# Kernel tuning notes

Measured on AMD Instinct MI355X. Metric: run time of the kernel, lower is better.

The kernel has to match this reference:

```python
import jax, jax.numpy as jnp
import numpy as np

N, HID, L, NC = 2048, 256, 4, 10
D0, D1, D2 = HID, HID // 2, HID // 8   # dims for degrees l=0,1,2
H, DH = 4, HID // 4                    # heads for degree-0 attention
F = D0 + D1 + D2                       # invariant feature width
C2 = float(np.sqrt(3.0))


def setup_inputs() -> dict:
    key = jax.random.key(0)
    ks = jax.random.split(key, 16)

    def w(k, shape, fan):
        return jax.random.normal(k, shape, jnp.float32) / np.float32(np.sqrt(fan))

    return {
        "x": jax.random.uniform(ks[0], (N, 118), jnp.float32),
        "pos": jax.random.normal(ks[1], (N, 3), jnp.float32) * 3.0,
        "emb_W": w(ks[2], (118, D0), 118),
        "emb_b": jnp.zeros((D0,), jnp.float32),
        "Wq": w(ks[3], (L, F, H * DH), F),
        "Wk": w(ks[4], (L, F, H * DH), F),
        "Wv0": w(ks[5], (L, D0, D0), D0),
        "Wv1": w(ks[6], (L, D1, D1), D1),
        "Wv2": w(ks[7], (L, D2, D2), D2),
        "Ws1": w(ks[8], (L, D0, D1), D0),
        "Ws2": w(ks[9], (L, D0, D2), D0),
        "Wffa": w(ks[10], (L, D0, 2 * D0), D0),
        "Wffb": w(ks[11], (L, 2 * D0, D0), 2 * D0),
        "Wg": w(ks[12], (L, F, D1 + D2), F),
        "out_W": w(ks[13], (D0, NC), D0),
        "out_b": jnp.zeros((NC,), jnp.float32),
    }


def _sph_harmonics(pos):
    """Real spherical harmonics Y1 [N,N,3], Y2 [N,N,5] of pairwise unit vectors."""
    rel = pos[None, :, :] - pos[:, None, :]                  # [N,N,3]
    dist = jnp.linalg.norm(rel, axis=-1, keepdims=True)
    valid = (dist > 1e-6).astype(pos.dtype)                  # zero out self-pairs
    u = rel / jnp.maximum(dist, 1e-6) * valid
    ux, uy, uz = u[..., 0], u[..., 1], u[..., 2]
    Y1 = u
    Y2 = jnp.stack([
        C2 * ux * uy,
        C2 * uy * uz,
        0.5 * (3.0 * uz * uz - 1.0),
        C2 * ux * uz,
        0.5 * C2 * (ux * ux - uy * uy),
    ], axis=-1) * valid                                      # [N,N,5]
    return Y1, Y2


def _invariants(x0, x1, x2):
    return jnp.concatenate([
        x0,
        jnp.linalg.norm(x1, axis=-1),
        jnp.linalg.norm(x2, axis=-1),
    ], axis=-1)                                              # [N,F]


def _layer(x0, x1, x2, Y1, Y2, Wq, Wk, Wv0, Wv1, Wv2, Ws1, Ws2, Wffa, Wffb, Wg):
    inv = _invariants(x0, x1, x2)
    q = (inv @ Wq).reshape(N, H, DH)
    k = (inv @ Wk).reshape(N, H, DH)
    attn = jax.nn.softmax(jnp.einsum('nhd,mhd->hnm', q, k) / np.float32(np.sqrt(DH)), axis=-1)

    # degree-0 aggregation (4 heads)
    v0 = (x0 @ Wv0).reshape(N, H, D0 // H)
    agg0 = jnp.einsum('hnm,mhc->nhc', attn, v0).reshape(N, D0)

    a = attn.mean(0)                                         # [N,N] single head for l>0
    # degree-1: channel-mixed values + degree-0 -> degree-1 via Y1
    v1 = jnp.einsum('mdc,de->mec', x1, Wv1)                  # [N,D1,3]
    agg1 = jnp.einsum('nm,mdc->ndc', a, v1)
    mix1 = jnp.einsum('nmc,md->ndc', a[:, :, None] * Y1, x0 @ Ws1)
    # degree-2: channel-mixed values + degree-0 -> degree-2 via Y2
    v2 = jnp.einsum('mdc,de->mec', x2, Wv2)                  # [N,D2,5]
    agg2 = jnp.einsum('nm,mdc->ndc', a, v2)
    mix2 = jnp.einsum('nmc,md->ndc', a[:, :, None] * Y2, x0 @ Ws2)

    x0 = x0 + agg0
    x1 = x1 + agg1 + mix1
    x2 = x2 + agg2 + mix2

    # gated equivariant feedforward
    x0 = x0 + jax.nn.silu(x0 @ Wffa) @ Wffb
    g = jax.nn.sigmoid(_invariants(x0, x1, x2) @ Wg)         # [N,D1+D2]
    x1 = x1 * g[:, :D1, None]
    x2 = x2 * g[:, D1:, None]
    return x0, x1, x2


def reference(x, pos, emb_W, emb_b, Wq, Wk, Wv0, Wv1, Wv2, Ws1, Ws2, Wffa, Wffb, Wg, out_W, out_b):
    Y1, Y2 = _sph_harmonics(pos)
    x0 = x @ emb_W + emb_b                                   # input embedding
    x1 = jnp.zeros((N, D1, 3), x0.dtype)
    x2 = jnp.zeros((N, D2, 5), x0.dtype)
    for l in range(L):
        x0, x1, x2 = _layer(x0, x1, x2, Y1, Y2,
                            Wq[l], Wk[l], Wv0[l], Wv1[l], Wv2[l],
                            Ws1[l], Ws2[l], Wffa[l], Wffb[l], Wg[l])
    return x0 @ out_W + out_b                                # [N, num_classes]
```

## Files before the change

kernel.cpp:

```cpp
#include <hip/hip_runtime.h>
#include <math.h>

#define N_    2048
#define D0_   256
#define D1_   128
#define D2_   32
#define F_    416
#define H_    4
#define DH_   64
#define L_    4
#define NC_   10
#define C2_   1.7320508075688772f
#define X12W  544

typedef unsigned short u16;
typedef __attribute__((ext_vector_type(8))) short short8v;
typedef __attribute__((ext_vector_type(4))) float f32x4;

union U8 { u16 u[8]; short8v v; };

__device__ __forceinline__ u16 f2bf(float f) {
    union { float f; unsigned int u; } x; x.f = f;
    unsigned int r = x.u + 0x7FFFu + ((x.u >> 16) & 1u);
    return (u16)(r >> 16);
}
__device__ __forceinline__ float bf2f(u16 u) {
    union { float f; unsigned int u; } x; x.u = ((unsigned int)u) << 16;
    return x.f;
}

__device__ __forceinline__ f32x4 mfma16(short8v a, short8v b, f32x4 c) {
    return __builtin_amdgcn_mfma_f32_16x16x32_bf16(a, b, c, 0, 0, 0);
}

enum { B_NN = 0, B_NT = 1 };
enum { EPI_STORE = 0, EPI_SILU = 1, EPI_SIGMOID = 2, EPI_ACCUM = 3, EPI_ATOMIC = 4,
       EPI_STOREB = 5 };

template<int BLAY, int EPI>
__global__ __launch_bounds__(256) void mfma_gemm(
    const float* __restrict__ A, int lda,
    const float* __restrict__ B, int ldb,
    const float* __restrict__ bias,
    float* __restrict__ C, int ldc,
    int M, int K, int Nn, float scale, int kchunk,
    int zk, long long Ah, long long Bh, long long Ch)
{
    __shared__ __align__(16) u16 As[64][40];
    __shared__ __align__(16) u16 Bs[64][40];
    const int t = threadIdx.x;
    const int bm = blockIdx.y * 64, bn = blockIdx.x * 64;
    const int hz = blockIdx.z / zk, kz = blockIdx.z % zk;
    A += (size_t)hz * Ah; B += (size_t)hz * Bh;
    const int lane = t & 63, w = t >> 6;
    const int r0 = (w >> 1) * 32, c0 = (w & 1) * 32;
    const int fr = lane & 15, fk = (lane >> 4) * 8;
    const int ml = t >> 2, k8 = (t & 3) * 8;
    const int kbeg = kz * kchunk;
    const int kend = (kbeg + kchunk < K) ? kbeg + kchunk : K;
    f32x4 acc[2][2] = {};

    for (int k0 = kbeg; k0 < kend; k0 += 32) {
        {
            U8 u;
            if (((lda & 3) == 0) && (k0 + 32 <= kend)) {
                const float* ap = A + (size_t)(bm + ml) * lda + k0 + k8;
                float4 a0 = *(const float4*)ap;
                float4 a1 = *(const float4*)(ap + 4);
                u.u[0]=f2bf(a0.x); u.u[1]=f2bf(a0.y); u.u[2]=f2bf(a0.z); u.u[3]=f2bf(a0.w);
                u.u[4]=f2bf(a1.x); u.u[5]=f2bf(a1.y); u.u[6]=f2bf(a1.z); u.u[7]=f2bf(a1.w);
            } else {
#pragma unroll
                for (int j = 0; j < 8; ++j) {
                    int kk = k0 + k8 + j;
                    u.u[j] = f2bf(kk < kend ? A[(size_t)(bm + ml) * lda + kk] : 0.f);
                }
            }
            *(short8v*)&As[ml][k8] = u.v;
        }
        {
            U8 u;
            if (BLAY == B_NT) {
                if (((ldb & 3) == 0) && (k0 + 32 <= kend) && (bn + ml < Nn)) {
                    const float* bp = B + (size_t)(bn + ml) * ldb + k0 + k8;
                    float4 b0 = *(const float4*)bp;
                    float4 b1 = *(const float4*)(bp + 4);
                    u.u[0]=f2bf(b0.x); u.u[1]=f2bf(b0.y); u.u[2]=f2bf(b0.z); u.u[3]=f2bf(b0.w);
                    u.u[4]=f2bf(b1.x); u.u[5]=f2bf(b1.y); u.u[6]=f2bf(b1.z); u.u[7]=f2bf(b1.w);
                } else {
#pragma unroll
                    for (int j = 0; j < 8; ++j) {
                        int kk = k0 + k8 + j;
                        u.u[j] = f2bf((kk < kend && bn + ml < Nn)
                                      ? B[(size_t)(bn + ml) * ldb + kk] : 0.f);
                    }
                }
            } else {
                int nc = bn + ml;
#pragma unroll
                for (int j = 0; j < 8; ++j) {
                    int kk = k0 + k8 + j;
                    u.u[j] = f2bf((kk < kend && nc < Nn) ? B[(size_t)kk * ldb + nc] : 0.f);
                }
            }
            *(short8v*)&Bs[ml][k8] = u.v;
        }
        __syncthreads();
        short8v a0 = *(const short8v*)&As[r0 + fr][fk];
        short8v a1 = *(const short8v*)&As[r0 + 16 + fr][fk];
        short8v b0 = *(const short8v*)&Bs[c0 + fr][fk];
        short8v b1 = *(const short8v*)&Bs[c0 + 16 + fr][fk];
        acc[0][0] = mfma16(a0, b0, acc[0][0]);
        acc[0][1] = mfma16(a0, b1, acc[0][1]);
        acc[1][0] = mfma16(a1, b0, acc[1][0]);
        acc[1][1] = mfma16(a1, b1, acc[1][1]);
        __syncthreads();
    }
#pragma unroll
    for (int mi = 0; mi < 2; ++mi)
#pragma unroll
    for (int ni = 0; ni < 2; ++ni)
#pragma unroll
    for (int r = 0; r < 4; ++r) {
        int row = bm + r0 + mi * 16 + ((lane >> 4) << 2) + r;
        int col = bn + c0 + ni * 16 + fr;
        if (col >= Nn) continue;
        float v = acc[mi][ni][r];
        if (EPI == EPI_STOREB) {
            ((u16*)C + (size_t)hz * Ch)[(size_t)row * ldc + col] = f2bf(v * scale);
        } else {
            float* cp = C + (size_t)hz * Ch + (size_t)row * ldc + col;
            if (EPI == EPI_STORE)   *cp = v * scale + (bias ? bias[col] : 0.f);
            if (EPI == EPI_SILU)    *cp = v / (1.f + expf(-v));
            if (EPI == EPI_SIGMOID) *cp = 1.f / (1.f + expf(-v));
            if (EPI == EPI_ACCUM)   *cp += v;
            if (EPI == EPI_ATOMIC)  atomicAdd(cp, v);
        }
    }
}

template<int NB, int EPI>
__global__ __launch_bounds__(256) void aggP(
    const u16* __restrict__ A, int lda,
    const float* __restrict__ B, int ldb,
    float* __restrict__ C, int ldc,
    int K, int Nn, int kchunk,
    int zk, long long Ah, long long Bh, long long Ch)
{
    __shared__ __align__(16) u16 As[64][40];
    __shared__ __align__(16) u16 Bs[NB][64][40];
    const int t = threadIdx.x;
    const int bm = blockIdx.y * 64, bn0 = blockIdx.x * 64 * NB;
    const int hz = blockIdx.z / zk, kz = blockIdx.z % zk;
    A += (size_t)hz * Ah; B += (size_t)hz * Bh; C += (size_t)hz * Ch;
    const int lane = t & 63, w = t >> 6;
    const int r0 = (w >> 1) * 32, c0 = (w & 1) * 32;
    const int fr = lane & 15, fk = (lane >> 4) * 8;
    const int ml = t >> 2, k8 = (t & 3) * 8;
    const int kbeg = kz * kchunk;
    const int kend = (kbeg + kchunk < K) ? kbeg + kchunk : K;
    f32x4 acc[NB][2][2] = {};

    for (int k0 = kbeg; k0 < kend; k0 += 32) {
        *(short8v*)&As[ml][k8] = *(const short8v*)(A + (size_t)(bm + ml) * lda + k0 + k8);
#pragma unroll
        for (int nb = 0; nb < NB; ++nb) {
            int nc = bn0 + nb * 64 + ml;
            U8 u;
#pragma unroll
            for (int j = 0; j < 8; ++j) {
                int kk = k0 + k8 + j;
                u.u[j] = f2bf(nc < Nn ? B[(size_t)kk * ldb + nc] : 0.f);
            }
            *(short8v*)&Bs[nb][ml][k8] = u.v;
        }
        __syncthreads();
        short8v a0 = *(const short8v*)&As[r0 + fr][fk];
        short8v a1 = *(const short8v*)&As[r0 + 16 + fr][fk];
#pragma unroll
        for (int nb = 0; nb < NB; ++nb) {
            short8v b0 = *(const short8v*)&Bs[nb][c0 + fr][fk];
            short8v b1 = *(const short8v*)&Bs[nb][c0 + 16 + fr][fk];
            acc[nb][0][0] = mfma16(a0, b0, acc[nb][0][0]);
            acc[nb][0][1] = mfma16(a0, b1, acc[nb][0][1]);
            acc[nb][1][0] = mfma16(a1, b0, acc[nb][1][0]);
            acc[nb][1][1] = mfma16(a1, b1, acc[nb][1][1]);
        }
        __syncthreads();
    }
#pragma unroll
    for (int nb = 0; nb < NB; ++nb)
#pragma unroll
    for (int mi = 0; mi < 2; ++mi)
#pragma unroll
    for (int ni = 0; ni < 2; ++ni)
#pragma unroll
    for (int r = 0; r < 4; ++r) {
        int row = bm + r0 + mi * 16 + ((lane >> 4) << 2) + r;
        int col = bn0 + nb * 64 + c0 + ni * 16 + fr;
        if (col >= Nn) continue;
        float v = acc[nb][mi][ni][r];
        float* cp = C + (size_t)row * ldc + col;
        if (EPI == EPI_ATOMIC) atomicAdd(cp, v);
        else                   *cp += v;
    }
}

__global__ void ucompute_kernel(const float* __restrict__ pos, u16* __restrict__ U) {
    int idx = blockIdx.x * 256 + threadIdx.x;
    int n = idx >> 11, m = idx & (N_ - 1);
    float rx = pos[m * 3 + 0] - pos[n * 3 + 0];
    float ry = pos[m * 3 + 1] - pos[n * 3 + 1];
    float rz = pos[m * 3 + 2] - pos[n * 3 + 2];
    float d2 = rx * rx + ry * ry + rz * rz;
    bool valid = d2 > 1e-12f;
    float rinv = valid ? rsqrtf(d2) : 0.f;
    size_t base = (size_t)n * N_ + m;
    const size_t CS = (size_t)N_ * N_;
    U[base]          = f2bf(rx * rinv);
    U[base + CS]     = f2bf(ry * rinv);
    U[base + 2 * CS] = f2bf(rz * rinv);
}

__global__ __launch_bounds__(256) void mixc_kernel(
    const u16* __restrict__ amb, const u16* __restrict__ U,
    const float* __restrict__ s1, const float* __restrict__ s2,
    float* __restrict__ x12)
{
    const int ch = blockIdx.z;
    const int gx = blockIdx.x;
    const int bm = blockIdx.y * 64;
    const size_t CS = (size_t)N_ * N_;
    const bool deg1 = ch < 3;
    const int colbase = deg1 ? (gx & 1) * 64 : 0;
    const int ks      = deg1 ? (gx >> 1) : gx;
    const int kchunk  = deg1 ? 512 : 256;
    const float* Bp   = deg1 ? s1 : s2;
    const int Bld     = deg1 ? 128 : 32;
    __shared__ __align__(16) u16 As[64][40];
    __shared__ __align__(16) u16 Bs[64][40];
    const int t = threadIdx.x, lane = t & 63, w = t >> 6;
    const int r0 = (w >> 1) * 32, c0 = (w & 1) * 32;
    const int fr = lane & 15, fk = (lane >> 4) * 8;
    const int ml = t >> 2, k8 = (t & 3) * 8;
    const int kbeg = ks * kchunk, kend = kbeg + kchunk;
    f32x4 acc[2][2] = {};

    for (int m0 = kbeg; m0 < kend; m0 += 32) {
        const size_t off = (size_t)(bm + ml) * N_ + m0 + k8;
        U8 am8; am8.v = *(const short8v*)(amb + off);
        U8 o;
        if (deg1) {
            U8 uv; uv.v = *(const short8v*)(U + (size_t)ch * CS + off);
#pragma unroll
            for (int j = 0; j < 8; ++j)
                o.u[j] = f2bf(bf2f(am8.u[j]) * bf2f(uv.u[j]));
        } else {
            U8 xv, yv, zv;
            xv.v = *(const short8v*)(U + off);
            yv.v = *(const short8v*)(U + CS + off);
            zv.v = *(const short8v*)(U + 2 * CS + off);
#pragma unroll
            for (int j = 0; j < 8; ++j) {
                float a = bf2f(am8.u[j]);
                float ux = bf2f(xv.u[j]), uy = bf2f(yv.u[j]), uz = bf2f(zv.u[j]);
                float y;
                if      (ch == 3) y = C2_ * ux * uy;
                else if (ch == 4) y = C2_ * uy * uz;
                else if (ch == 5) y = (ux*ux + uy*uy + uz*uz > 0.5f)
                                      ? 0.5f * (3.f * uz * uz - 1.f) : 0.f;
                else if (ch == 6) y = C2_ * ux * uz;
                else              y = 0.5f * C2_ * (ux * ux - uy * uy);
                o.u[j] = f2bf(a * y);
            }
        }
        *(short8v*)&As[ml][k8] = o.v;
        {
            int nc = colbase + ml;
            U8 u;
#pragma unroll
            for (int j = 0; j < 8; ++j)
                u.u[j] = f2bf((deg1 || nc < 32)
                              ? Bp[(size_t)(m0 + k8 + j) * Bld + nc] : 0.f);
            *(short8v*)&Bs[ml][k8] = u.v;
        }
        __syncthreads();
        short8v a0 = *(const short8v*)&As[r0 + fr][fk];
        short8v a1 = *(const short8v*)&As[r0 + 16 + fr][fk];
        short8v b0 = *(const short8v*)&Bs[c0 + fr][fk];
        short8v b1 = *(const short8v*)&Bs[c0 + 16 + fr][fk];
        acc[0][0] = mfma16(a0, b0, acc[0][0]);
        acc[0][1] = mfma16(a0, b1, acc[0][1]);
        acc[1][0] = mfma16(a1, b0, acc[1][0]);
        acc[1][1] = mfma16(a1, b1, acc[1][1]);
        __syncthreads();
    }
#pragma unroll
    for (int mi = 0; mi < 2; ++mi)
#pragma unroll
    for (int ni = 0; ni < 2; ++ni)
#pragma unroll
    for (int r = 0; r < 4; ++r) {
        int row = bm + r0 + mi * 16 + ((lane >> 4) << 2) + r;
        int col = colbase + c0 + ni * 16 + fr;
        float v = acc[mi][ni][r];
        if (deg1)          atomicAdd(&x12[(size_t)row * X12W + col * 3 + ch], v);
        else if (col < 32) atomicAdd(&x12[(size_t)row * X12W + 384 + col * 5 + (ch - 3)], v);
    }
}

__global__ void invar_kernel(const float* __restrict__ x0, const float* __restrict__ x12,
                             float* __restrict__ inv) {
    int n = blockIdx.x, t = threadIdx.x;
    inv[(size_t)n * F_ + t] = x0[(size_t)n * D0_ + t];
    if (t < 128) {
        const float* p = x12 + (size_t)n * X12W + t * 3;
        inv[(size_t)n * F_ + 256 + t] = sqrtf(p[0]*p[0] + p[1]*p[1] + p[2]*p[2]);
    }
    if (t < 32) {
        const float* p = x12 + (size_t)n * X12W + 384 + t * 5;
        inv[(size_t)n * F_ + 384 + t] =
            sqrtf(p[0]*p[0] + p[1]*p[1] + p[2]*p[2] + p[3]*p[3] + p[4]*p[4]);
    }
}

__global__ void v1_kernel(const float* __restrict__ x12, const float* __restrict__ W,
                          float* __restrict__ Vflat) {
    int m = blockIdx.x, t = threadIdx.x;
    __shared__ float sh[384];
    sh[t] = x12[(size_t)m * X12W + t];
    __syncthreads();
    int e = t / 3, c = t % 3;
    float acc = 0.f;
#pragma unroll 4
    for (int d = 0; d < 128; ++d)
        acc = fmaf(sh[d * 3 + c], W[d * 128 + e], acc);
    Vflat[(size_t)m * X12W + t] = acc;
}

__global__ void v2_kernel(const float* __restrict__ x12, const float* __restrict__ W,
                          float* __restrict__ Vflat) {
    int m = blockIdx.x, t = threadIdx.x;
    __shared__ float sh[160];
    if (t < 160) sh[t] = x12[(size_t)m * X12W + 384 + t];
    __syncthreads();
    if (t < 160) {
        int e = t / 5, c = t % 5;
        float acc = 0.f;
#pragma unroll 4
        for (int d = 0; d < 32; ++d)
            acc = fmaf(sh[d * 5 + c], W[d * 32 + e], acc);
        Vflat[(size_t)m * X12W + 384 + t] = acc;
    }
}

__global__ void softmax4(u16* __restrict__ Sb, u16* __restrict__ amb) {
    int n = blockIdx.x, t = threadIdx.x;
    __shared__ float red[256];
    const size_t NN = (size_t)N_ * N_;
    float amv[8] = {};
    for (int h = 0; h < H_; ++h) {
        u16* Sp = Sb + (size_t)h * NN + (size_t)n * N_ + t * 8;
        U8 sv; sv.v = *(const short8v*)Sp;
        float s[8];
#pragma unroll
        for (int j = 0; j < 8; ++j) s[j] = bf2f(sv.u[j]);
        float mx = s[0];
#pragma unroll
        for (int j = 1; j < 8; ++j) mx = fmaxf(mx, s[j]);
        red[t] = mx; __syncthreads();
        for (int st = 128; st > 0; st >>= 1) { if (t < st) red[t] = fmaxf(red[t], red[t + st]); __syncthreads(); }
        mx = red[0]; __syncthreads();
        float sum = 0.f;
#pragma unroll
        for (int j = 0; j < 8; ++j) { s[j] = expf(s[j] - mx); sum += s[j]; }
        red[t] = sum; __syncthreads();
        for (int st = 128; st > 0; st >>= 1) { if (t < st) red[t] += red[t + st]; __syncthreads(); }
        float rinv = 1.f / red[0]; __syncthreads();
        U8 pv;
#pragma unroll
        for (int j = 0; j < 8; ++j) {
            float p = s[j] * rinv;
            pv.u[j] = f2bf(p);
            amv[j] += 0.25f * p;
        }
        *(short8v*)Sp = pv.v;
    }
    U8 av;
#pragma unroll
    for (int j = 0; j < 8; ++j) av.u[j] = f2bf(amv[j]);
    *(short8v*)(amb + (size_t)n * N_ + t * 8) = av.v;
}

__global__ void gate_kernel(const float* __restrict__ g, float* __restrict__ x12) {
    int idx = blockIdx.x * 256 + threadIdx.x;
    if (idx >= N_ * X12W) return;
    int n = idx / X12W, j = idx % X12W;
    float gv = (j < 384) ? g[n * 160 + j / 3] : g[n * 160 + 128 + (j - 384) / 5];
    x12[idx] *= gv;
}

extern "C" void kernel_launch(void* const* d_in, const int* in_sizes, int n_in,
                              void* d_out, int out_size, void* d_ws, size_t ws_size,
                              hipStream_t stream) {
    const float* x    = (const float*)d_in[0];
    const float* pos  = (const float*)d_in[1];
    const float* embW = (const float*)d_in[2];
    const float* embB = (const float*)d_in[3];
    const float* Wq   = (const float*)d_in[4];
    const float* Wk   = (const float*)d_in[5];
    const float* Wv0  = (const float*)d_in[6];
    const float* Wv1  = (const float*)d_in[7];
    const float* Wv2  = (const float*)d_in[8];
    const float* Ws1  = (const float*)d_in[9];
    const float* Ws2  = (const float*)d_in[10];
    const float* Wffa = (const float*)d_in[11];
    const float* Wffb = (const float*)d_in[12];
    const float* Wg   = (const float*)d_in[13];
    const float* outW = (const float*)d_in[14];
    const float* outB = (const float*)d_in[15];
    float* out = (float*)d_out;

    const size_t NN = (size_t)N_ * N_;
    float* p = (float*)d_ws;
    float* x0    = p; p += N_ * D0_;
    float* x12   = p; p += N_ * X12W;
    float* inv   = p; p += N_ * F_;
    float* q     = p; p += N_ * D0_;
    float* k     = p; p += N_ * D0_;
    float* v0    = p; p += N_ * D0_;
    float* Vflat = p; p += N_ * X12W;
    float* s1    = p; p += N_ * D1_;
    float* s2    = p; p += N_ * D2_;
    float* fft   = p; p += N_ * 512;
    float* gm    = p; p += N_ * 160;
    u16* ub  = (u16*)p;
    u16* Sb  = ub; ub += 4 * NN;
    u16* amb = ub; ub += NN;
    u16* U   = ub;

    hipMemsetAsync(x12, 0, (size_t)N_ * X12W * sizeof(float), stream);
    ucompute_kernel<<<(N_ * N_) / 256, 256, 0, stream>>>(pos, U);

    mfma_gemm<B_NN, EPI_STORE><<<dim3(4, 32), 256, 0, stream>>>(
        x, 118, embW, 256, embB, x0, 256, N_, 118, 256, 1.f, 118, 1, 0, 0, 0);

    for (int l = 0; l < L_; ++l) {
        const float* Wq_l   = Wq   + (size_t)l * F_ * 256;
        const float* Wk_l   = Wk   + (size_t)l * F_ * 256;
        const float* Wv0_l  = Wv0  + (size_t)l * 256 * 256;
        const float* Wv1_l  = Wv1  + (size_t)l * 128 * 128;
        const float* Wv2_l  = Wv2  + (size_t)l * 32 * 32;
        const float* Ws1_l  = Ws1  + (size_t)l * 256 * 128;
        const float* Ws2_l  = Ws2  + (size_t)l * 256 * 32;
        const float* Wffa_l = Wffa + (size_t)l * 256 * 512;
        const float* Wffb_l = Wffb + (size_t)l * 512 * 256;
        const float* Wg_l   = Wg   + (size_t)l * F_ * 160;

        invar_kernel<<<N_, 256, 0, stream>>>(x0, x12, inv);
        mfma_gemm<B_NN, EPI_STORE><<<dim3(4, 32), 256, 0, stream>>>(
            inv, F_, Wq_l, 256, nullptr, q, 256, N_, F_, 256, 1.f, F_, 1, 0, 0, 0);
        mfma_gemm<B_NN, EPI_STORE><<<dim3(4, 32), 256, 0, stream>>>(
            inv, F_, Wk_l, 256, nullptr, k, 256, N_, F_, 256, 1.f, F_, 1, 0, 0, 0);
        mfma_gemm<B_NN, EPI_STORE><<<dim3(4, 32), 256, 0, stream>>>(
            x0, 256, Wv0_l, 256, nullptr, v0, 256, N_, 256, 256, 1.f, 256, 1, 0, 0, 0);
        mfma_gemm<B_NN, EPI_STORE><<<dim3(2, 32), 256, 0, stream>>>(
            x0, 256, Ws1_l, 128, nullptr, s1, 128, N_, 256, 128, 1.f, 256, 1, 0, 0, 0);
        mfma_gemm<B_NN, EPI_STORE><<<dim3(1, 32), 256, 0, stream>>>(
            x0, 256, Ws2_l, 32, nullptr, s2, 32, N_, 256, 32, 1.f, 256, 1, 0, 0, 0);
        v1_kernel<<<N_, 384, 0, stream>>>(x12, Wv1_l, Vflat);
        v2_kernel<<<N_, 192, 0, stream>>>(x12, Wv2_l, Vflat);

        mfma_gemm<B_NT, EPI_STOREB><<<dim3(32, 32, 4), 256, 0, stream>>>(
            q, 256, k, 256, nullptr, (float*)Sb, N_, N_, 64, N_, 0.125f, 64,
            1, 64, 64, (long long)NN);
        softmax4<<<N_, 256, 0, stream>>>(Sb, amb);
        aggP<1, EPI_ATOMIC><<<dim3(1, 32, 32), 256, 0, stream>>>(
            Sb, N_, v0, 256, x0, 256, N_, 64, 256,
            8, (long long)NN, 64, 64);

        aggP<3, EPI_ATOMIC><<<dim3(3, 32, 4), 256, 0, stream>>>(
            amb, N_, Vflat, X12W, x12, X12W, N_, X12W, 512,
            4, 0, 0, 0);
        mixc_kernel<<<dim3(8, 32, 8), 256, 0, stream>>>(amb, U, s1, s2, x12);

        mfma_gemm<B_NN, EPI_SILU><<<dim3(8, 32), 256, 0, stream>>>(
            x0, 256, Wffa_l, 512, nullptr, fft, 512, N_, 256, 512, 1.f, 256, 1, 0, 0, 0);
        mfma_gemm<B_NN, EPI_ACCUM><<<dim3(4, 32), 256, 0, stream>>>(
            fft, 512, Wffb_l, 256, nullptr, x0, 256, N_, 512, 256, 1.f, 512, 1, 0, 0, 0);

        invar_kernel<<<N_, 256, 0, stream>>>(x0, x12, inv);
        mfma_gemm<B_NN, EPI_SIGMOID><<<dim3(3, 32), 256, 0, stream>>>(
            inv, F_, Wg_l, 160, nullptr, gm, 160, N_, F_, 160, 1.f, F_, 1, 0, 0, 0);
        gate_kernel<<<(N_ * X12W + 255) / 256, 256, 0, stream>>>(gm, x12);
    }

    mfma_gemm<B_NN, EPI_STORE><<<dim3(1, 32), 256, 0, stream>>>(
        x0, 256, outW, NC_, outB, out, NC_, N_, 256, NC_, 1.f, 256, 1, 0, 0, 0);
}
```

Before: 1.569 ms.

## Pre-transpose B operands to bf16 and stage mix results in contiguous accumulators

Adds a bf16 transpose kernel so the aggregation and mix GEMMs load their B tiles as contiguous 16-byte vectors instead of eight strided fp32 loads with per-element conversion. The mix kernel now writes atomics to a channel-separated contiguous buffer rather than strided interleaved x12 slots, then a combine kernel adds that buffer into x12. The degree-1 mix grid is also split further along K (16 x-blocks, 256-wide chunks). The cost is extra transpose, memset and combine launches plus more atomic traffic from the finer K split.

```diff
diff --git a/kernel.cpp b/kernel.cpp
--- a/kernel.cpp
+++ b/kernel.cpp
@@ -139,10 +139,30 @@
     }
 }
 
-template<int NB, int EPI>
+__global__ __launch_bounds__(256) void transpose_bf16(
+    const float* __restrict__ in, u16* __restrict__ outT, int R, int C)
+{
+    __shared__ float tile[64][65];
+    const int br = blockIdx.y * 64, bc = blockIdx.x * 64;
+    const int t = threadIdx.x, lc = t & 63, q = t >> 6;
+#pragma unroll 4
+    for (int r = 0; r < 16; ++r) {
+        int row = br + q * 16 + r, col = bc + lc;
+        tile[q * 16 + r][lc] = (col < C) ? in[(size_t)row * C + col] : 0.f;
+    }
+    __syncthreads();
+#pragma unroll 4
+    for (int r = 0; r < 16; ++r) {
+        int orow = bc + q * 16 + r;
+        int ocol = br + lc;
+        if (orow < C) outT[(size_t)orow * R + ocol] = f2bf(tile[lc][q * 16 + r]);
+    }
+}
+
+template<int NB>
 __global__ __launch_bounds__(256) void aggP(
     const u16* __restrict__ A, int lda,
-    const float* __restrict__ B, int ldb,
+    const u16* __restrict__ BT, int ldk,
     float* __restrict__ C, int ldc,
     int K, int Nn, int kchunk,
     int zk, long long Ah, long long Bh, long long Ch)
@@ -152,7 +172,7 @@
     const int t = threadIdx.x;
     const int bm = blockIdx.y * 64, bn0 = blockIdx.x * 64 * NB;
     const int hz = blockIdx.z / zk, kz = blockIdx.z % zk;
-    A += (size_t)hz * Ah; B += (size_t)hz * Bh; C += (size_t)hz * Ch;
+    A += (size_t)hz * Ah; BT += (size_t)hz * Bh; C += (size_t)hz * Ch;
     const int lane = t & 63, w = t >> 6;
     const int r0 = (w >> 1) * 32, c0 = (w & 1) * 32;
     const int fr = lane & 15, fk = (lane >> 4) * 8;
@@ -166,13 +186,9 @@
 #pragma unroll
         for (int nb = 0; nb < NB; ++nb) {
             int nc = bn0 + nb * 64 + ml;
-            U8 u;
-#pragma unroll
-            for (int j = 0; j < 8; ++j) {
-                int kk = k0 + k8 + j;
-                u.u[j] = f2bf(nc < Nn ? B[(size_t)kk * ldb + nc] : 0.f);
-            }
-            *(short8v*)&Bs[nb][ml][k8] = u.v;
+            short8v z = {};
+            *(short8v*)&Bs[nb][ml][k8] = (nc < Nn)
+                ? *(const short8v*)(BT + (size_t)nc * ldk + k0 + k8) : z;
         }
         __syncthreads();
         short8v a0 = *(const short8v*)&As[r0 + fr][fk];
@@ -199,10 +215,7 @@
         int row = bm + r0 + mi * 16 + ((lane >> 4) << 2) + r;
         int col = bn0 + nb * 64 + c0 + ni * 16 + fr;
         if (col >= Nn) continue;
-        float v = acc[nb][mi][ni][r];
-        float* cp = C + (size_t)row * ldc + col;
-        if (EPI == EPI_ATOMIC) atomicAdd(cp, v);
-        else                   *cp += v;
+        atomicAdd(C + (size_t)row * ldc + col, acc[nb][mi][ni][r]);
     }
 }
 
@@ -224,26 +237,25 @@
 
 __global__ __launch_bounds__(256) void mixc_kernel(
     const u16* __restrict__ amb, const u16* __restrict__ U,
-    const float* __restrict__ s1, const float* __restrict__ s2,
-    float* __restrict__ x12)
+    const u16* __restrict__ s1T, const u16* __restrict__ s2T,
+    float* __restrict__ Macc)
 {
     const int ch = blockIdx.z;
     const int gx = blockIdx.x;
+    const bool deg1 = ch < 3;
+    if (!deg1 && gx >= 8) return;
     const int bm = blockIdx.y * 64;
     const size_t CS = (size_t)N_ * N_;
-    const bool deg1 = ch < 3;
     const int colbase = deg1 ? (gx & 1) * 64 : 0;
     const int ks      = deg1 ? (gx >> 1) : gx;
-    const int kchunk  = deg1 ? 512 : 256;
-    const float* Bp   = deg1 ? s1 : s2;
-    const int Bld     = deg1 ? 128 : 32;
+    const u16* BT     = deg1 ? s1T : s2T;
     __shared__ __align__(16) u16 As[64][40];
     __shared__ __align__(16) u16 Bs[64][40];
     const int t = threadIdx.x, lane = t & 63, w = t >> 6;
     const int r0 = (w >> 1) * 32, c0 = (w & 1) * 32;
     const int fr = lane & 15, fk = (lane >> 4) * 8;
     const int ml = t >> 2, k8 = (t & 3) * 8;
-    const int kbeg = ks * kchunk, kend = kbeg + kchunk;
+    const int kbeg = ks * 256, kend = kbeg + 256;
     f32x4 acc[2][2] = {};
 
     for (int m0 = kbeg; m0 < kend; m0 += 32) {
@@ -277,12 +289,9 @@
         *(short8v*)&As[ml][k8] = o.v;
         {
             int nc = colbase + ml;
-            U8 u;
-#pragma unroll
-            for (int j = 0; j < 8; ++j)
-                u.u[j] = f2bf((deg1 || nc < 32)
-                              ? Bp[(size_t)(m0 + k8 + j) * Bld + nc] : 0.f);
-            *(short8v*)&Bs[ml][k8] = u.v;
+            short8v z = {};
+            *(short8v*)&Bs[ml][k8] = (deg1 || nc < 32)
+                ? *(const short8v*)(BT + (size_t)nc * N_ + m0 + k8) : z;
         }
         __syncthreads();
         short8v a0 = *(const short8v*)&As[r0 + fr][fk];
@@ -304,9 +313,28 @@
         int row = bm + r0 + mi * 16 + ((lane >> 4) << 2) + r;
         int col = colbase + c0 + ni * 16 + fr;
         float v = acc[mi][ni][r];
-        if (deg1)          atomicAdd(&x12[(size_t)row * X12W + col * 3 + ch], v);
-        else if (col < 32) atomicAdd(&x12[(size_t)row * X12W + 384 + col * 5 + (ch - 3)], v);
-    }
+        if (deg1)
+            atomicAdd(&Macc[(size_t)ch * N_ * 128 + (size_t)row * 128 + col], v);
+        else if (col < 32)
+            atomicAdd(&Macc[(size_t)3 * N_ * 128 + (size_t)(ch - 3) * N_ * 32
+                            + (size_t)row * 32 + col], v);
+    }
+}
+
+__global__ void mix_combine(const float* __restrict__ Macc, float* __restrict__ x12) {
+    int idx = blockIdx.x * 256 + threadIdx.x;
+    if (idx >= N_ * X12W) return;
+    int n = idx / X12W, j = idx % X12W;
+    float v;
+    if (j < 384) {
+        int e = j / 3, c = j - 3 * e;
+        v = Macc[(size_t)c * N_ * 128 + (size_t)n * 128 + e];
+    } else {
+        int jj = j - 384;
+        int e = jj / 5, c = jj - 5 * e;
+        v = Macc[(size_t)3 * N_ * 128 + (size_t)c * N_ * 32 + (size_t)n * 32 + e];
+    }
+    x12[idx] += v;
 }
 
 __global__ void invar_kernel(const float* __restrict__ x0, const float* __restrict__ x12,
@@ -434,10 +462,15 @@
     float* s2    = p; p += N_ * D2_;
     float* fft   = p; p += N_ * 512;
     float* gm    = p; p += N_ * 160;
-    u16* ub  = (u16*)p;
-    u16* Sb  = ub; ub += 4 * NN;
-    u16* amb = ub; ub += NN;
-    u16* U   = ub;
+    float* Macc  = p; p += 3 * N_ * 128 + 5 * N_ * 32;
+    u16* ub   = (u16*)p;
+    u16* Sb   = ub; ub += 4 * NN;
+    u16* amb  = ub; ub += NN;
+    u16* U    = ub; ub += 3 * NN;
+    u16* v0T  = ub; ub += D0_ * N_;
+    u16* s1T  = ub; ub += D1_ * N_;
+    u16* s2T  = ub; ub += D2_ * N_;
+    u16* VflatT = ub; ub += X12W * N_;
 
     hipMemsetAsync(x12, 0, (size_t)N_ * X12W * sizeof(float), stream);
     ucompute_kernel<<<(N_ * N_) / 256, 256, 0, stream>>>(pos, U);
@@ -457,6 +490,7 @@
         const float* Wffb_l = Wffb + (size_t)l * 512 * 256;
         const float* Wg_l   = Wg   + (size_t)l * F_ * 160;
 
+        hipMemsetAsync(Macc, 0, (3 * N_ * 128 + 5 * N_ * 32) * sizeof(float), stream);
         invar_kernel<<<N_, 256, 0, stream>>>(x0, x12, inv);
         mfma_gemm<B_NN, EPI_STORE><<<dim3(4, 32), 256, 0, stream>>>(
             inv, F_, Wq_l, 256, nullptr, q, 256, N_, F_, 256, 1.f, F_, 1, 0, 0, 0);
@@ -471,18 +505,24 @@
         v1_kernel<<<N_, 384, 0, stream>>>(x12, Wv1_l, Vflat);
         v2_kernel<<<N_, 192, 0, stream>>>(x12, Wv2_l, Vflat);
 
+        transpose_bf16<<<dim3(4, 32), 256, 0, stream>>>(v0, v0T, N_, 256);
+        transpose_bf16<<<dim3(2, 32), 256, 0, stream>>>(s1, s1T, N_, 128);
+        transpose_bf16<<<dim3(1, 32), 256, 0, stream>>>(s2, s2T, N_, 32);
+        transpose_bf16<<<dim3(9, 32), 256, 0, stream>>>(Vflat, VflatT, N_, X12W);
+
         mfma_gemm<B_NT, EPI_STOREB><<<dim3(32, 32, 4), 256, 0, stream>>>(
             q, 256, k, 256, nullptr, (float*)Sb, N_, N_, 64, N_, 0.125f, 64,
             1, 64, 64, (long long)NN);
         softmax4<<<N_, 256, 0, stream>>>(Sb, amb);
-        aggP<1, EPI_ATOMIC><<<dim3(1, 32, 32), 256, 0, stream>>>(
-            Sb, N_, v0, 256, x0, 256, N_, 64, 256,
-            8, (long long)NN, 64, 64);
-
-        aggP<3, EPI_ATOMIC><<<dim3(3, 32, 4), 256, 0, stream>>>(
-            amb, N_, Vflat, X12W, x12, X12W, N_, X12W, 512,
+        aggP<1><<<dim3(1, 32, 32), 256, 0, stream>>>(
+            Sb, N_, v0T, N_, x0, 256, N_, 64, 256,
+            8, (long long)NN, (long long)(64 * N_), 64);
+
+        aggP<3><<<dim3(3, 32, 4), 256, 0, stream>>>(
+            amb, N_, VflatT, N_, x12, X12W, N_, X12W, 512,
             4, 0, 0, 0);
-        mixc_kernel<<<dim3(8, 32, 8), 256, 0, stream>>>(amb, U, s1, s2, x12);
+        mixc_kernel<<<dim3(16, 32, 8), 256, 0, stream>>>(amb, U, s1T, s2T, Macc);
+        mix_combine<<<(N_ * X12W + 255) / 256, 256, 0, stream>>>(Macc, x12);
 
         mfma_gemm<B_NN, EPI_SILU><<<dim3(8, 32), 256, 0, stream>>>(
             x0, 256, Wffa_l, 512, nullptr, fft, 512, N_, 256, 512, 1.f, 256, 1, 0, 0, 0);
```

After: 1.484 ms. 5.4% less time.
